# Optimization experiments

Measured on AMD Instinct MI355X. Metric: run time of the kernel, lower is better.

The kernel has to match this reference:

```python
import jax, jax.numpy as jnp
import numpy as np

# Static feature-pyramid shapes (stride 8/16/32 of a 512x512 image)
SPATIAL_SHAPES = ((64, 64), (32, 32), (16, 16))
SEQ = sum(h * w for h, w in SPATIAL_SHAPES)  # 5376
B, D, NH, NL, NP = 4, 256, 8, 3, 4
DH = D // NH  # 32


def _reference_points():
    # normalized pixel centers per level, valid_ratios == 1
    refs = []
    for (h, w) in SPATIAL_SHAPES:
        ry = (jnp.arange(h, dtype=jnp.float32) + 0.5) / h
        rx = (jnp.arange(w, dtype=jnp.float32) + 0.5) / w
        yy, xx = jnp.meshgrid(ry, rx, indexing='ij')
        refs.append(jnp.stack([xx.reshape(-1), yy.reshape(-1)], -1))  # [h*w, 2]
    ref = jnp.concatenate(refs, 0)  # [S, 2]
    return jnp.broadcast_to(ref[None, :, None, :], (B, SEQ, NL, 2))


def setup_inputs() -> dict:
    key = jax.random.key(0)
    ks = jax.random.split(key, 8)
    s = 0.02
    return {
        'hidden_states': jax.random.normal(ks[0], (B, SEQ, D), jnp.float32),
        'position_embeddings': jax.random.normal(ks[1], (B, SEQ, D), jnp.float32),
        'reference_points': _reference_points(),
        'Wv': jax.random.normal(ks[2], (D, D), jnp.float32) * s,
        'bv': jnp.zeros((D,), jnp.float32),
        'Wo': jax.random.normal(ks[3], (D, NH * NL * NP * 2), jnp.float32) * s,
        'bo': jax.random.normal(ks[4], (NH * NL * NP * 2,), jnp.float32) * 0.1,
        'Wa': jax.random.normal(ks[5], (D, NH * NL * NP), jnp.float32) * s,
        'ba': jnp.zeros((NH * NL * NP,), jnp.float32),
        'Wout': jax.random.normal(ks[6], (D, D), jnp.float32) * s,
        'bout': jnp.zeros((D,), jnp.float32),
    }


def _bilinear_sample(img, gx, gy):
    # img: [N, C, H, W]; gx, gy: [N, Q, P] in [-1, 1]
    # grid_sample(mode='bilinear', padding_mode='zeros', align_corners=False)
    N, C, H, W = img.shape
    x = (gx + 1.0) * (W * 0.5) - 0.5
    y = (gy + 1.0) * (H * 0.5) - 0.5
    x0 = jnp.floor(x)
    y0 = jnp.floor(y)
    wx, wy = x - x0, y - y0
    flat = img.reshape(N, C, H * W)
    out = jnp.zeros((N, C) + gx.shape[1:], img.dtype)
    for xi, wxi in ((x0, 1.0 - wx), (x0 + 1.0, wx)):
        for yi, wyi in ((y0, 1.0 - wy), (y0 + 1.0, wy)):
            valid = (xi >= 0) & (xi < W) & (yi >= 0) & (yi < H)
            xc = jnp.clip(xi, 0, W - 1).astype(jnp.int32)
            yc = jnp.clip(yi, 0, H - 1).astype(jnp.int32)
            idx = (yc * W + xc).reshape(N, 1, -1)  # [N,1,Q*P]
            v = jnp.take_along_axis(flat, idx, axis=2).reshape(N, C, *gx.shape[1:])
            out = out + v * (wxi * wyi * valid.astype(img.dtype))[:, None]
    return out  # [N, C, Q, P]


def reference(hidden_states, position_embeddings, reference_points,
              Wv, bv, Wo, bo, Wa, ba, Wout, bout):
    hs = hidden_states + position_embeddings  # queries carry pos embed
    value = hidden_states @ Wv + bv           # value from raw encoder states
    value = value.reshape(B, SEQ, NH, DH)

    off = (hs @ Wo + bo).reshape(B, SEQ, NH, NL, NP, 2)
    attn = jax.nn.softmax((hs @ Wa + ba).reshape(B, SEQ, NH, NL * NP), -1)
    attn = attn.reshape(B, SEQ, NH, NL, NP)

    # offset normalizer: [W_l, H_l] per level
    norm = jnp.array([[w, h] for (h, w) in SPATIAL_SHAPES], jnp.float32)
    loc = reference_points[:, :, None, :, None, :] + off / norm[None, None, None, :, None, :]
    grid = 2.0 * loc - 1.0  # [B, Q, H, L, P, 2]

    sampled = []
    start = 0
    for lvl, (h, w) in enumerate(SPATIAL_SHAPES):
        v_l = value[:, start:start + h * w]  # [B, h*w, H, d]
        start += h * w
        v_l = v_l.transpose(0, 2, 3, 1).reshape(B * NH, DH, h, w)
        g_l = grid[:, :, :, lvl].transpose(0, 2, 1, 3, 4).reshape(B * NH, SEQ, NP, 2)
        sampled.append(_bilinear_sample(v_l, g_l[..., 0], g_l[..., 1]))  # [B*H,d,Q,P]
    sampled = jnp.stack(sampled, -2).reshape(B * NH, DH, SEQ, NL * NP)

    aw = attn.transpose(0, 2, 1, 3, 4).reshape(B * NH, 1, SEQ, NL * NP)
    out = (sampled * aw).sum(-1)                   # [B*H, d, Q]
    out = out.reshape(B, NH * DH, SEQ).transpose(0, 2, 1)  # [B, Q, D]
    out = out @ Wout + bout
    return out, attn
```

## Files before the change

kernel.cpp:

```cpp
#include <hip/hip_runtime.h>
#include <hip/hip_bf16.h>
#include <math.h>

#define BB 4
#define SEQ 5376
#define DD 256
#define NH 8
#define NL 3
#define NP 4
#define DH 32
#define MTOT (BB * SEQ)

typedef __attribute__((ext_vector_type(8))) short bf16x8;
typedef __attribute__((ext_vector_type(4))) float f32x4;
typedef __attribute__((ext_vector_type(2))) float f32x2;

#define GLD_LDS16(src, dst) __builtin_amdgcn_global_load_lds( \
    (const __attribute__((address_space(1))) void*)(src),     \
    (__attribute__((address_space(3))) void*)(dst), 16, 0, 0)

__device__ __forceinline__ ushort f2b(float f) {
    __hip_bfloat16 h = __float2bfloat16(f);
    return *reinterpret_cast<ushort*>(&h);
}

__global__ __launch_bounds__(256) void prep_all(
    const float* __restrict__ hidden, const float* __restrict__ pos,
    const float* __restrict__ Wv, const float* __restrict__ Wo,
    const float* __restrict__ Wa, const float* __restrict__ Wout,
    const float* __restrict__ bo, const float* __restrict__ ba,
    ushort4* __restrict__ hb, ushort4* __restrict__ hsb,
    ushort* __restrict__ Wt, float* __restrict__ bcomb, int n4) {
    int bid = blockIdx.x;
    int tid = threadIdx.x;
    if (bid <= 800) {
        if (bid == 800) {
            for (int i = tid; i < 288; i += 256)
                bcomb[i] = (i < 192) ? bo[i] : ba[i - 192];
            return;
        }
        int row = bid;
        const float* src;
        int N, n;
        if (row < 256)      { src = Wv;   N = 256; n = row; }
        else if (row < 448) { src = Wo;   N = 192; n = row - 256; }
        else if (row < 544) { src = Wa;   N = 96;  n = row - 448; }
        else                { src = Wout; N = 256; n = row - 544; }
        float v = src[(size_t)tid * N + n];
        Wt[(size_t)row * 256 + tid] = f2b(v);
        return;
    }
    const float4* h4 = (const float4*)hidden;
    const float4* p4 = (const float4*)pos;
    int i = (bid - 801) * 256 + tid;
    int stride = (gridDim.x - 801) * 256;
    for (; i < n4; i += stride) {
        float4 a = h4[i], b = p4[i];
        ushort4 ua, us;
        ua.x = f2b(a.x); ua.y = f2b(a.y); ua.z = f2b(a.z); ua.w = f2b(a.w);
        us.x = f2b(a.x + b.x); us.y = f2b(a.y + b.y);
        us.z = f2b(a.z + b.z); us.w = f2b(a.w + b.w);
        hb[i] = ua;
        hsb[i] = us;
    }
}

__global__ __launch_bounds__(256) void gemm_dual(
    const ushort* __restrict__ hb, const ushort* __restrict__ hsb,
    const ushort* __restrict__ Wv_t, const ushort* __restrict__ Wcomb_t,
    const float* __restrict__ bv, const float* __restrict__ bcomb,
    ushort* __restrict__ value_bf, float* __restrict__ comb) {
    const int K = 256, BK = 64;
    __shared__ ushort As[128 * 64];
    __shared__ ushort Bs[128 * 64];

    int b = blockIdx.x;
    const ushort* A;
    const ushort* W;
    const float* bias;
    int bn, bm, N;
    bool obf;
    if (b < 336) {
        A = hb;  W = Wv_t;    bias = bv;    N = 256; obf = true;
        bn = (b & 1) * 128;   bm = (b >> 1) * 128;
    } else {
        int bb = b - 336;
        A = hsb; W = Wcomb_t; bias = bcomb; N = 288; obf = false;
        bn = (bb % 3) * 128;  bm = (bb / 3) * 128;
    }

    int tid = threadIdx.x;
    int lane = tid & 63;
    int wid = tid >> 6;
    int wr = wid >> 1, wc = wid & 1;
    int lr = lane & 15;
    int kg = lane >> 4;

    f32x4 acc[4][4] = {};

    for (int k0 = 0; k0 < K; k0 += BK) {
        #pragma unroll
        for (int c = 0; c < 4; c++) {
            int e = tid + 256 * c;
            int row = e >> 3;
            int ch = e & 7;
            int gch = ch ^ (row & 7);
            GLD_LDS16(A + (size_t)(bm + row) * K + k0 + 8 * gch, &As[e * 8]);
            GLD_LDS16(W + (size_t)(bn + row) * K + k0 + 8 * gch, &Bs[e * 8]);
        }
        __syncthreads();
        #pragma unroll
        for (int ks = 0; ks < 2; ks++) {
            bf16x8 af[4], bfr[4];
            #pragma unroll
            for (int mf = 0; mf < 4; mf++) {
                int R = wr * 64 + mf * 16 + lr;
                int sc = (ks * 4 + kg) ^ (R & 7);
                af[mf] = *(bf16x8*)&As[R * 64 + sc * 8];
            }
            #pragma unroll
            for (int nf = 0; nf < 4; nf++) {
                int R = wc * 64 + nf * 16 + lr;
                int sc = (ks * 4 + kg) ^ (R & 7);
                bfr[nf] = *(bf16x8*)&Bs[R * 64 + sc * 8];
            }
            #pragma unroll
            for (int mf = 0; mf < 4; mf++)
                #pragma unroll
                for (int nf = 0; nf < 4; nf++)
                    acc[mf][nf] = __builtin_amdgcn_mfma_f32_16x16x32_bf16(
                        af[mf], bfr[nf], acc[mf][nf], 0, 0, 0);
        }
        __syncthreads();
    }

    #pragma unroll
    for (int nf = 0; nf < 4; nf++) {
        int gc = bn + wc * 64 + nf * 16 + lr;
        if (gc >= N) continue;
        float bvv = bias[gc];
        #pragma unroll
        for (int mf = 0; mf < 4; mf++) {
            int gr0 = bm + wr * 64 + mf * 16 + kg * 4;
            #pragma unroll
            for (int r = 0; r < 4; r++) {
                float v = acc[mf][nf][r] + bvv;
                if (obf) {
                    int hh = gc >> 5, cc = gc & 31;
                    value_bf[(size_t)hh * ((size_t)MTOT * 32)
                             + (size_t)(gr0 + r) * 32 + cc] = f2b(v);
                } else {
                    comb[(size_t)(gr0 + r) * 288 + gc] = v;
                }
            }
        }
    }
}

__global__ __launch_bounds__(256) void gemm_out(
    const ushort* __restrict__ A, const ushort* __restrict__ Wt,
    const float* __restrict__ bias, float* __restrict__ C) {
    const int K = 256, BK = 64;
    __shared__ ushort As[128 * 64];
    __shared__ ushort Bs[64 * 64];
    int bm = blockIdx.y * 128;
    int bn = blockIdx.x * 64;
    int tid = threadIdx.x;
    int lane = tid & 63;
    int wid = tid >> 6;
    int wr = wid >> 1, wc = wid & 1;
    int lr = lane & 15;
    int kg = lane >> 4;

    f32x4 acc[4][2] = {};

    for (int k0 = 0; k0 < K; k0 += BK) {
        #pragma unroll
        for (int c = 0; c < 4; c++) {
            int e = tid + 256 * c;
            int row = e >> 3;
            int ch = e & 7;
            int gch = ch ^ (row & 7);
            GLD_LDS16(A + (size_t)(bm + row) * K + k0 + 8 * gch, &As[e * 8]);
        }
        #pragma unroll
        for (int c = 0; c < 2; c++) {
            int e = tid + 256 * c;
            int row = e >> 3;
            int ch = e & 7;
            int gch = ch ^ (row & 7);
            GLD_LDS16(Wt + (size_t)(bn + row) * K + k0 + 8 * gch, &Bs[e * 8]);
        }
        __syncthreads();
        #pragma unroll
        for (int ks = 0; ks < 2; ks++) {
            bf16x8 af[4], bfr[2];
            #pragma unroll
            for (int mf = 0; mf < 4; mf++) {
                int R = wr * 64 + mf * 16 + lr;
                int sc = (ks * 4 + kg) ^ (R & 7);
                af[mf] = *(bf16x8*)&As[R * 64 + sc * 8];
            }
            #pragma unroll
            for (int nf = 0; nf < 2; nf++) {
                int R = wc * 32 + nf * 16 + lr;
                int sc = (ks * 4 + kg) ^ (R & 7);
                bfr[nf] = *(bf16x8*)&Bs[R * 64 + sc * 8];
            }
            #pragma unroll
            for (int mf = 0; mf < 4; mf++)
                #pragma unroll
                for (int nf = 0; nf < 2; nf++)
                    acc[mf][nf] = __builtin_amdgcn_mfma_f32_16x16x32_bf16(
                        af[mf], bfr[nf], acc[mf][nf], 0, 0, 0);
        }
        __syncthreads();
    }

    #pragma unroll
    for (int nf = 0; nf < 2; nf++) {
        int gc = bn + wc * 32 + nf * 16 + lr;
        float bvv = bias[gc];
        #pragma unroll
        for (int mf = 0; mf < 4; mf++) {
            int gr0 = bm + wr * 64 + mf * 16 + kg * 4;
            #pragma unroll
            for (int r = 0; r < 4; r++) {
                C[(size_t)(gr0 + r) * 256 + gc] = acc[mf][nf][r] + bvv;
            }
        }
    }
}

__device__ __forceinline__ void fma8p(f32x2 acc[4], float wt, uint4 u) {
    f32x2 w2 = {wt, wt};
    f32x2 v0, v1, v2, v3;
    v0[0] = __uint_as_float(u.x << 16); v0[1] = __uint_as_float(u.x & 0xffff0000u);
    v1[0] = __uint_as_float(u.y << 16); v1[1] = __uint_as_float(u.y & 0xffff0000u);
    v2[0] = __uint_as_float(u.z << 16); v2[1] = __uint_as_float(u.z & 0xffff0000u);
    v3[0] = __uint_as_float(u.w << 16); v3[1] = __uint_as_float(u.w & 0xffff0000u);
    acc[0] = __builtin_elementwise_fma(v0, w2, acc[0]);
    acc[1] = __builtin_elementwise_fma(v1, w2, acc[1]);
    acc[2] = __builtin_elementwise_fma(v2, w2, acc[2]);
    acc[3] = __builtin_elementwise_fma(v3, w2, acc[3]);
}

__global__ __launch_bounds__(128) void msda_sample_v12(
    const ushort* __restrict__ value, const float* __restrict__ comb,
    const float* __restrict__ refp, float* __restrict__ attn_out,
    ushort* __restrict__ out) {
    __shared__ int2   s_idx[2][8][13];
    __shared__ float4 s_w[2][8][13];
    int tid = threadIdx.x;
    int bq0 = blockIdx.x * 2;

    #pragma unroll
    for (int it = 0; it < 2; it++) {
        int t = tid + it * 128;
        int lp = t & 15;
        int qh = t >> 4;
        int q = qh >> 3, h = qh & 7;
        int bq = bq0 + q;
        bool active = lp < 12;
        const float* crow = comb + (size_t)bq * 288;
        float logit = active ? crow[192 + h * 12 + lp] : -INFINITY;
        float m = logit;
        m = fmaxf(m, __shfl_xor(m, 1, 16));
        m = fmaxf(m, __shfl_xor(m, 2, 16));
        m = fmaxf(m, __shfl_xor(m, 4, 16));
        m = fmaxf(m, __shfl_xor(m, 8, 16));
        float e = active ? expf(logit - m) : 0.f;
        float s = e;
        s += __shfl_xor(s, 1, 16);
        s += __shfl_xor(s, 2, 16);
        s += __shfl_xor(s, 4, 16);
        s += __shfl_xor(s, 8, 16);
        float aw = e / s;
        if (active) {
            attn_out[(size_t)bq * 96 + h * 12 + lp] = aw;
            int l = lp >> 2;
            int b = bq / SEQ;
            int Wl = 64 >> l;
            float fW = (float)Wl;
            float rx = refp[(size_t)bq * 6 + 2 * l];
            float ry = refp[(size_t)bq * 6 + 2 * l + 1];
            float ox = crow[h * 24 + lp * 2];
            float oy = crow[h * 24 + lp * 2 + 1];
            float x = rx * fW + ox - 0.5f;
            float y = ry * fW + oy - 0.5f;
            float x0f = floorf(x), y0f = floorf(y);
            float wx = x - x0f, wy = y - y0f;
            int x0 = (int)x0f, y0 = (int)y0f;
            int x1 = x0 + 1, y1 = y0 + 1;
            float vx0 = (x0 >= 0 && x0 < Wl) ? 1.f : 0.f;
            float vx1 = (x1 >= 0 && x1 < Wl) ? 1.f : 0.f;
            float vy0 = (y0 >= 0 && y0 < Wl) ? 1.f : 0.f;
            float vy1 = (y1 >= 0 && y1 < Wl) ? 1.f : 0.f;
            int yc0 = min(max(y0, 0), Wl - 1);
            int yc1 = min(max(y1, 0), Wl - 1);
            int px = min(max(x0, 0), Wl - 2);
            float wxl = (1.f - wx) * vx0;
            float wxh = wx * vx1;
            float wA, wB;
            if (px == x0)      { wA = wxl; wB = wxh; }
            else if (px == x1) { wA = wxh; wB = 0.f; }
            else               { wA = 0.f; wB = wxl; }
            float wy0v = aw * (1.f - wy) * vy0;
            float wy1v = aw * wy * vy1;
            int st = (l == 0) ? 0 : ((l == 1) ? 4096 : 5120);
            int rowbase = b * SEQ + st;
            s_idx[q][h][lp] = make_int2((rowbase + yc0 * Wl + px) * 32,
                                        (rowbase + yc1 * Wl + px) * 32);
            s_w[q][h][lp] = make_float4(wA * wy0v, wB * wy0v,
                                        wA * wy1v, wB * wy1v);
        }
    }
    __syncthreads();

    int wave = tid >> 6, lane = tid & 63;
    int q = wave;
    int bq = bq0 + q;
    int h = lane >> 3;
    int d8 = lane & 7;
    int part = d8 >> 2;
    int c4 = d8 & 3;
    const ushort* vb = value + (size_t)h * ((size_t)MTOT * 32)
                       + part * 32 + c4 * 8;

    f32x2 acc[4] = {{0.f, 0.f}, {0.f, 0.f}, {0.f, 0.f}, {0.f, 0.f}};
    #pragma unroll
    for (int lp = 0; lp < 12; lp++) {
        int2 ii = s_idx[q][h][lp];
        float4 ww = s_w[q][h][lp];
        float w0 = part ? ww.y : ww.x;
        float w1 = part ? ww.w : ww.z;
        uint4 u0 = *(const uint4*)(vb + ii.x);
        uint4 u1 = *(const uint4*)(vb + ii.y);
        fma8p(acc, w0, u0);
        fma8p(acc, w1, u1);
    }

    #pragma unroll
    for (int i = 0; i < 4; i++) {
        acc[i][0] += __shfl_xor(acc[i][0], 4);
        acc[i][1] += __shfl_xor(acc[i][1], 4);
    }
    if (part == 0) {
        bf16x8 o;
        o[0] = (short)f2b(acc[0][0]); o[1] = (short)f2b(acc[0][1]);
        o[2] = (short)f2b(acc[1][0]); o[3] = (short)f2b(acc[1][1]);
        o[4] = (short)f2b(acc[2][0]); o[5] = (short)f2b(acc[2][1]);
        o[6] = (short)f2b(acc[3][0]); o[7] = (short)f2b(acc[3][1]);
        *(bf16x8*)(out + (size_t)bq * 256 + h * 32 + c4 * 8) = o;
    }
}

extern "C" void kernel_launch(void* const* d_in, const int* in_sizes, int n_in,
                              void* d_out, int out_size, void* d_ws, size_t ws_size,
                              hipStream_t stream) {
    const float* hidden = (const float*)d_in[0];
    const float* pos    = (const float*)d_in[1];
    const float* refp   = (const float*)d_in[2];
    const float* Wv     = (const float*)d_in[3];
    const float* bv     = (const float*)d_in[4];
    const float* Wo     = (const float*)d_in[5];
    const float* bo     = (const float*)d_in[6];
    const float* Wa     = (const float*)d_in[7];
    const float* ba     = (const float*)d_in[8];
    const float* Wout   = (const float*)d_in[9];
    const float* bout   = (const float*)d_in[10];

    float* out      = (float*)d_out;
    float* attn_out = out + (size_t)BB * SEQ * DD;

    const size_t BSD = (size_t)BB * SEQ * DD;
    char* w = (char*)d_ws;
    ushort* value_bf = (ushort*)w;  w += BSD * 2;
    float*  comb     = (float*)w;   w += (size_t)MTOT * 288 * 4;
    ushort* sampb    = (ushort*)w;  w += BSD * 2;
    ushort* hb       = (ushort*)w;  w += BSD * 2;
    ushort* hsb      = (ushort*)w;  w += BSD * 2;
    ushort* Wt       = (ushort*)w;  w += (size_t)800 * 256 * 2;
    float*  bcomb    = (float*)w;

    {
        int n4 = (int)(BSD / 4);
        prep_all<<<801 + 2048, 256, 0, stream>>>(hidden, pos, Wv, Wo, Wa, Wout,
                                                 bo, ba, (ushort4*)hb, (ushort4*)hsb,
                                                 Wt, bcomb, n4);
    }

    const ushort* Wv_t    = Wt;
    const ushort* Wcomb_t = Wt + (size_t)256 * 256;
    const ushort* Wout_t  = Wt + (size_t)544 * 256;

    gemm_dual<<<840, 256, 0, stream>>>(hb, hsb, Wv_t, Wcomb_t, bv, bcomb,
                                       value_bf, comb);

    msda_sample_v12<<<MTOT / 2, 128, 0, stream>>>(value_bf, comb, refp,
                                                  attn_out, sampb);

    {
        dim3 grid(DD / 64, MTOT / 128);
        gemm_out<<<grid, 256, 0, stream>>>(sampb, Wout_t, bout, out);
    }
}
```

Before: 78.21 us.

## Stage coarsest-level value map in LDS with per-head query-chunk blocks

The sampling kernel is reorganised so each block handles one (batch, 256-query chunk, head). For that head it loads the whole 16x16 level-2 value map into shared memory with async global-to-LDS loads, then reads that level's bilinear corners from LDS instead of global memory. Per-query softmax and corner setup now run in four 64-query sub-chunks with barriers between them. This cuts global gathers and improves head locality, but the grid drops from about 10.7k small blocks to 672 larger ones, which may hurt occupancy and latency hiding.

```diff
diff --git a/kernel.cpp b/kernel.cpp
--- a/kernel.cpp
+++ b/kernel.cpp
@@ -245,113 +245,146 @@
     acc[3] = __builtin_elementwise_fma(v3, w2, acc[3]);
 }
 
-__global__ __launch_bounds__(128) void msda_sample_v12(
+__global__ __launch_bounds__(256) void msda_sample_v13(
     const ushort* __restrict__ value, const float* __restrict__ comb,
     const float* __restrict__ refp, float* __restrict__ attn_out,
     ushort* __restrict__ out) {
-    __shared__ int2   s_idx[2][8][13];
-    __shared__ float4 s_w[2][8][13];
+    __shared__ ushort l2s[256 * 32];
+    __shared__ int2   s_idx[64][13];
+    __shared__ float4 s_w[64][13];
     int tid = threadIdx.x;
-    int bq0 = blockIdx.x * 2;
-
-    #pragma unroll
-    for (int it = 0; it < 2; it++) {
-        int t = tid + it * 128;
-        int lp = t & 15;
-        int qh = t >> 4;
-        int q = qh >> 3, h = qh & 7;
-        int bq = bq0 + q;
-        bool active = lp < 12;
-        const float* crow = comb + (size_t)bq * 288;
-        float logit = active ? crow[192 + h * 12 + lp] : -INFINITY;
-        float m = logit;
-        m = fmaxf(m, __shfl_xor(m, 1, 16));
-        m = fmaxf(m, __shfl_xor(m, 2, 16));
-        m = fmaxf(m, __shfl_xor(m, 4, 16));
-        m = fmaxf(m, __shfl_xor(m, 8, 16));
-        float e = active ? expf(logit - m) : 0.f;
-        float s = e;
-        s += __shfl_xor(s, 1, 16);
-        s += __shfl_xor(s, 2, 16);
-        s += __shfl_xor(s, 4, 16);
-        s += __shfl_xor(s, 8, 16);
-        float aw = e / s;
-        if (active) {
-            attn_out[(size_t)bq * 96 + h * 12 + lp] = aw;
-            int l = lp >> 2;
-            int b = bq / SEQ;
-            int Wl = 64 >> l;
-            float fW = (float)Wl;
-            float rx = refp[(size_t)bq * 6 + 2 * l];
-            float ry = refp[(size_t)bq * 6 + 2 * l + 1];
-            float ox = crow[h * 24 + lp * 2];
-            float oy = crow[h * 24 + lp * 2 + 1];
-            float x = rx * fW + ox - 0.5f;
-            float y = ry * fW + oy - 0.5f;
-            float x0f = floorf(x), y0f = floorf(y);
-            float wx = x - x0f, wy = y - y0f;
-            int x0 = (int)x0f, y0 = (int)y0f;
-            int x1 = x0 + 1, y1 = y0 + 1;
-            float vx0 = (x0 >= 0 && x0 < Wl) ? 1.f : 0.f;
-            float vx1 = (x1 >= 0 && x1 < Wl) ? 1.f : 0.f;
-            float vy0 = (y0 >= 0 && y0 < Wl) ? 1.f : 0.f;
-            float vy1 = (y1 >= 0 && y1 < Wl) ? 1.f : 0.f;
-            int yc0 = min(max(y0, 0), Wl - 1);
-            int yc1 = min(max(y1, 0), Wl - 1);
-            int px = min(max(x0, 0), Wl - 2);
-            float wxl = (1.f - wx) * vx0;
-            float wxh = wx * vx1;
-            float wA, wB;
-            if (px == x0)      { wA = wxl; wB = wxh; }
-            else if (px == x1) { wA = wxh; wB = 0.f; }
-            else               { wA = 0.f; wB = wxl; }
-            float wy0v = aw * (1.f - wy) * vy0;
-            float wy1v = aw * wy * vy1;
-            int st = (l == 0) ? 0 : ((l == 1) ? 4096 : 5120);
-            int rowbase = b * SEQ + st;
-            s_idx[q][h][lp] = make_int2((rowbase + yc0 * Wl + px) * 32,
-                                        (rowbase + yc1 * Wl + px) * 32);
-            s_w[q][h][lp] = make_float4(wA * wy0v, wB * wy0v,
-                                        wA * wy1v, wB * wy1v);
-        }
-    }
-    __syncthreads();
+    int blk = blockIdx.x;
+    int h     = blk & 7;
+    int rest  = blk >> 3;
+    int chunk = rest % 21;
+    int b     = rest / 21;
+    int bq0 = b * SEQ + chunk * 256;
+
+    {
+        const ushort* l2src = value + (size_t)h * ((size_t)MTOT * 32)
+                              + ((size_t)b * SEQ + 5120) * 32;
+        #pragma unroll
+        for (int c = 0; c < 4; c++) {
+            int e = tid + 256 * c;
+            GLD_LDS16(l2src + e * 8, &l2s[e * 8]);
+        }
+    }
 
     int wave = tid >> 6, lane = tid & 63;
-    int q = wave;
-    int bq = bq0 + q;
-    int h = lane >> 3;
+    int q8 = lane >> 3;
     int d8 = lane & 7;
     int part = d8 >> 2;
     int c4 = d8 & 3;
-    const ushort* vb = value + (size_t)h * ((size_t)MTOT * 32)
-                       + part * 32 + c4 * 8;
-
-    f32x2 acc[4] = {{0.f, 0.f}, {0.f, 0.f}, {0.f, 0.f}, {0.f, 0.f}};
-    #pragma unroll
-    for (int lp = 0; lp < 12; lp++) {
-        int2 ii = s_idx[q][h][lp];
-        float4 ww = s_w[q][h][lp];
-        float w0 = part ? ww.y : ww.x;
-        float w1 = part ? ww.w : ww.z;
-        uint4 u0 = *(const uint4*)(vb + ii.x);
-        uint4 u1 = *(const uint4*)(vb + ii.y);
-        fma8p(acc, w0, u0);
-        fma8p(acc, w1, u1);
-    }
-
-    #pragma unroll
-    for (int i = 0; i < 4; i++) {
-        acc[i][0] += __shfl_xor(acc[i][0], 4);
-        acc[i][1] += __shfl_xor(acc[i][1], 4);
-    }
-    if (part == 0) {
-        bf16x8 o;
-        o[0] = (short)f2b(acc[0][0]); o[1] = (short)f2b(acc[0][1]);
-        o[2] = (short)f2b(acc[1][0]); o[3] = (short)f2b(acc[1][1]);
-        o[4] = (short)f2b(acc[2][0]); o[5] = (short)f2b(acc[2][1]);
-        o[6] = (short)f2b(acc[3][0]); o[7] = (short)f2b(acc[3][1]);
-        *(bf16x8*)(out + (size_t)bq * 256 + h * 32 + c4 * 8) = o;
+    const ushort* vbg = value + (size_t)h * ((size_t)MTOT * 32)
+                        + part * 32 + c4 * 8;
+    int lofs = part * 32 + c4 * 8;
+
+    for (int cc = 0; cc < 4; cc++) {
+        int q0 = cc * 64;
+        #pragma unroll
+        for (int it = 0; it < 4; it++) {
+            int t = tid + it * 256;
+            int lp = t & 15;
+            int q6 = t >> 4;
+            int bq = bq0 + q0 + q6;
+            bool active = lp < 12;
+            const float* crow = comb + (size_t)bq * 288;
+            float logit = active ? crow[192 + h * 12 + lp] : -INFINITY;
+            float m = logit;
+            m = fmaxf(m, __shfl_xor(m, 1, 16));
+            m = fmaxf(m, __shfl_xor(m, 2, 16));
+            m = fmaxf(m, __shfl_xor(m, 4, 16));
+            m = fmaxf(m, __shfl_xor(m, 8, 16));
+            float e = active ? expf(logit - m) : 0.f;
+            float s = e;
+            s += __shfl_xor(s, 1, 16);
+            s += __shfl_xor(s, 2, 16);
+            s += __shfl_xor(s, 4, 16);
+            s += __shfl_xor(s, 8, 16);
+            float aw = e / s;
+            if (active) {
+                attn_out[(size_t)bq * 96 + h * 12 + lp] = aw;
+                int l = lp >> 2;
+                int Wl = 64 >> l;
+                float fW = (float)Wl;
+                float rx = refp[(size_t)bq * 6 + 2 * l];
+                float ry = refp[(size_t)bq * 6 + 2 * l + 1];
+                float ox = crow[h * 24 + lp * 2];
+                float oy = crow[h * 24 + lp * 2 + 1];
+                float x = rx * fW + ox - 0.5f;
+                float y = ry * fW + oy - 0.5f;
+                float x0f = floorf(x), y0f = floorf(y);
+                float wx = x - x0f, wy = y - y0f;
+                int x0 = (int)x0f, y0 = (int)y0f;
+                int x1 = x0 + 1, y1 = y0 + 1;
+                float vx0 = (x0 >= 0 && x0 < Wl) ? 1.f : 0.f;
+                float vx1 = (x1 >= 0 && x1 < Wl) ? 1.f : 0.f;
+                float vy0 = (y0 >= 0 && y0 < Wl) ? 1.f : 0.f;
+                float vy1 = (y1 >= 0 && y1 < Wl) ? 1.f : 0.f;
+                int yc0 = min(max(y0, 0), Wl - 1);
+                int yc1 = min(max(y1, 0), Wl - 1);
+                int px = min(max(x0, 0), Wl - 2);
+                float wxl = (1.f - wx) * vx0;
+                float wxh = wx * vx1;
+                float wA, wB;
+                if (px == x0)      { wA = wxl; wB = wxh; }
+                else if (px == x1) { wA = wxh; wB = 0.f; }
+                else               { wA = 0.f; wB = wxl; }
+                float wy0v = aw * (1.f - wy) * vy0;
+                float wy1v = aw * wy * vy1;
+                int r0 = yc0 * Wl + px;
+                int r1 = yc1 * Wl + px;
+                if (l == 2) {
+                    s_idx[q6][lp] = make_int2(r0 * 32, r1 * 32);
+                } else {
+                    int st = (l == 0) ? 0 : 4096;
+                    int rowbase = b * SEQ + st;
+                    s_idx[q6][lp] = make_int2((rowbase + r0) * 32,
+                                              (rowbase + r1) * 32);
+                }
+                s_w[q6][lp] = make_float4(wA * wy0v, wB * wy0v,
+                                          wA * wy1v, wB * wy1v);
+            }
+        }
+        __syncthreads();
+
+        #pragma unroll
+        for (int p = 0; p < 2; p++) {
+            int q6 = wave * 16 + p * 8 + q8;
+            int bq = bq0 + q0 + q6;
+            f32x2 acc[4] = {{0.f, 0.f}, {0.f, 0.f}, {0.f, 0.f}, {0.f, 0.f}};
+            #pragma unroll
+            for (int lp = 0; lp < 12; lp++) {
+                int2 ii = s_idx[q6][lp];
+                float4 ww = s_w[q6][lp];
+                float w0 = part ? ww.y : ww.x;
+                float w1 = part ? ww.w : ww.z;
+                uint4 u0, u1;
+                if (lp >= 8) {
+                    u0 = *(const uint4*)&l2s[lofs + ii.x];
+                    u1 = *(const uint4*)&l2s[lofs + ii.y];
+                } else {
+                    u0 = *(const uint4*)(vbg + ii.x);
+                    u1 = *(const uint4*)(vbg + ii.y);
+                }
+                fma8p(acc, w0, u0);
+                fma8p(acc, w1, u1);
+            }
+            #pragma unroll
+            for (int i = 0; i < 4; i++) {
+                acc[i][0] += __shfl_xor(acc[i][0], 4);
+                acc[i][1] += __shfl_xor(acc[i][1], 4);
+            }
+            if (part == 0) {
+                bf16x8 o;
+                o[0] = (short)f2b(acc[0][0]); o[1] = (short)f2b(acc[0][1]);
+                o[2] = (short)f2b(acc[1][0]); o[3] = (short)f2b(acc[1][1]);
+                o[4] = (short)f2b(acc[2][0]); o[5] = (short)f2b(acc[2][1]);
+                o[6] = (short)f2b(acc[3][0]); o[7] = (short)f2b(acc[3][1]);
+                *(bf16x8*)(out + (size_t)bq * 256 + h * 32 + c4 * 8) = o;
+            }
+        }
+        __syncthreads();
     }
 }
 
@@ -397,8 +430,8 @@
     gemm_dual<<<840, 256, 0, stream>>>(hb, hsb, Wv_t, Wcomb_t, bv, bcomb,
                                        value_bf, comb);
 
-    msda_sample_v12<<<MTOT / 2, 128, 0, stream>>>(value_bf, comb, refp,
-                                                  attn_out, sampb);
+    msda_sample_v13<<<672, 256, 0, stream>>>(value_bf, comb, refp,
+                                             attn_out, sampb);
 
     {
         dim3 grid(DD / 64, MTOT / 128);
```

After: 89.78 us. +14.8%, slower.
